# Performance work log

Hardware: AMD Instinct MI355X
Metric: run time of the kernel (lower is better)

## Reference

```python
import jax, jax.numpy as jnp
import numpy as np

N, D, S, R = 50000, 256, 6, 4
EPS = 1e-5

def group_norm1(x, w, b):
    # GroupNorm with 1 group on [N, C]: normalize each row over channels
    m = jnp.mean(x, axis=-1, keepdims=True)
    v = jnp.mean(jnp.square(x - m), axis=-1, keepdims=True)
    return (x - m) * jax.lax.rsqrt(v + EPS) * w + b

def setup_inputs() -> dict:
    key = jax.random.key(0)
    ks = jax.random.split(key, 10)
    scale = 1.0 / np.sqrt(D)
    return {
        'lane_features': jax.random.normal(ks[0], (N, D), jnp.float32),
        'W_ctr': jax.random.normal(ks[1], (R, D, D), jnp.float32) * scale,
        'norm_w': jnp.ones((R, D), jnp.float32),
        'norm_b': jnp.zeros((R, D), jnp.float32),
        'W_ctr2': jax.random.normal(ks[2], (R, D, D), jnp.float32) * scale,
        'ctr2_norm_w': jnp.ones((R, D), jnp.float32),
        'ctr2_norm_b': jnp.zeros((R, D), jnp.float32),
        'W_pre': jax.random.normal(ks[3], (R, S, D, D), jnp.float32) * scale,
        'W_suc': jax.random.normal(ks[4], (R, S, D, D), jnp.float32) * scale,
        'pre_idx': jax.random.randint(ks[5], (S, N), 0, N, jnp.int32),
        'suc_idx': jax.random.randint(ks[6], (S, N), 0, N, jnp.int32),
        'n_hop_pre': jax.random.randint(ks[7], (S, N), 0, N, jnp.int32),
        'n_hop_suc': jax.random.randint(ks[8], (S, N), 0, N, jnp.int32),
    }

def reference(lane_features, W_ctr, norm_w, norm_b, W_ctr2, ctr2_norm_w,
              ctr2_norm_b, W_pre, W_suc, pre_idx, suc_idx, n_hop_pre, n_hop_suc):
    x = lane_features
    res = x
    for i in range(R):
        # ctr linear (bias=False): x @ W.T
        temp = x @ W_ctr[i].T
        for k in range(S):
            # pre branch: gather n_hop_pre, linear, scatter-add at suc
            msg_pre = x[n_hop_pre[k]] @ W_pre[i, k].T
            temp = temp.at[suc_idx[k]].add(msg_pre)
            # suc branch: gather n_hop_suc, linear, scatter-add at pre
            msg_suc = x[n_hop_suc[k]] @ W_suc[i, k].T
            temp = temp.at[pre_idx[k]].add(msg_suc)
        x = jax.nn.relu(group_norm1(temp, norm_w[i], norm_b[i]))
        # ctr2: Linear(no bias) + GroupNorm, no activation
        x = group_norm1(x @ W_ctr2[i].T, ctr2_norm_w[i], ctr2_norm_b[i])
        x = jax.nn.relu(x + res)
        res = x
    return x
```

## Files before the change

### kernel.cpp

```cpp
#include <hip/hip_runtime.h>

#define NROWS 50000
#define DIM   256
#define SHOPS 6
#define ROUNDS 4
#define EPSV  1e-5f
#define ND ((size_t)NROWS * DIM)
#define NB  196
#define EMAXR 32768
#define EMAXND ((size_t)EMAXR * DIM)

typedef _Float16 f16x8 __attribute__((ext_vector_type(8)));
typedef _Float16 f16x4 __attribute__((ext_vector_type(4)));
typedef float    f32x4 __attribute__((ext_vector_type(4)));

#define GLDS16(GP, LP) \
    __builtin_amdgcn_global_load_lds((const __attribute__((address_space(1))) unsigned*)(GP), \
                                     (__attribute__((address_space(3))) unsigned*)(LP), 16, 0, 0)

__device__ __forceinline__ int imin(int a, int b) { return a < b ? a : b; }

__global__ __launch_bounds__(256)
void gemm_p(const _Float16* __restrict__ A, const _Float16* __restrict__ WH,
            int s0, int s1, int nz, _Float16* __restrict__ C0,
            _Float16* __restrict__ CZ, int ctr0, int nwg,
            const int* __restrict__ LIVE, const int* __restrict__ Ecnt,
            int sbase)
{
    __shared__ _Float16 lds[3][8192];
    char* ldsb = (char*)lds;

    const int bid = blockIdx.x;
    const int q   = nwg >> 3, r = nwg & 7;
    const int xcd = bid & 7,  ii = bid >> 3;
    const int g   = (xcd < r) ? xcd * (q + 1) + ii
                              : r * (q + 1) + (xcd - r) * q + ii;
    const int j   = g / (2 * nz);
    const int sub = g - j * 2 * nz;
    const int by  = sub & 1;
    const size_t z = sub >> 1;
    int xp, jj;
    if (j < 7 * 49) { xp = j / 49; jj = j % 49; }
    else            { xp = 7; jj = j - 7 * 49; }
    const int bx = jj * 8 + xp;

    const int seg = sbase + (int)z;
    const int En  = (seg >= 0) ? Ecnt[seg] : NROWS;
    const int bm0 = bx * 128;
    if (bm0 >= En) return;
    const int* lvp = (seg >= 0) ? LIVE + (size_t)seg * NROWS : nullptr;

    const int tid = threadIdx.x;
    const int l   = tid & 63;
    const int w   = tid >> 6;
    const int wm  = w & 1;
    const int wn  = w >> 1;
    const int bn0 = by * 128;
    const int lr  = l & 15;
    const int sl  = l >> 4;

    const int wslot = (z == 0) ? s0 : s1 + (int)z;
    const char* Ab = (const char*)A;
    const char* Wb = (const char*)(WH + (size_t)wslot * (DIM * DIM));

    int arow[2], slog[2], wrow[2];
    #pragma unroll
    for (int qq = 0; qq < 2; ++qq) {
        const int c   = (w * 2 + qq) * 64 + l;
        const int row = c >> 2;
        slog[qq] = (c & 3) ^ ((row >> 1) & 3);
        const int cl = imin(bm0 + row, En - 1);
        arow[qq] = lvp ? lvp[cl] : cl;
        wrow[qq] = bn0 + row;
    }

    f32x4 acc[4][4];
    #pragma unroll
    for (int mt = 0; mt < 4; ++mt)
        #pragma unroll
        for (int nt = 0; nt < 4; ++nt)
            acc[mt][nt] = (f32x4){0.f, 0.f, 0.f, 0.f};

    auto stage = [&](int step, int buf) {
        const int kt64 = step * 64;
        char* base = ldsb + buf * 16384;
        #pragma unroll
        for (int qq = 0; qq < 2; ++qq) {
            GLDS16(Ab + (size_t)arow[qq] * 512 + kt64 + slog[qq] * 16,
                   base + (w * 2 + qq) * 1024);
            GLDS16(Wb + (size_t)wrow[qq] * 512 + kt64 + slog[qq] * 16,
                   base + 8192 + (w * 2 + qq) * 1024);
        }
    };

    auto compute = [&](int buf) {
        const char* base = ldsb + buf * 16384;
        f16x8 af[4], bf[4];
        #pragma unroll
        for (int mt = 0; mt < 4; ++mt) {
            const int row = wm * 64 + mt * 16 + lr;
            af[mt] = *(const f16x8*)(base + row * 64 + ((sl ^ ((row >> 1) & 3)) << 4));
        }
        #pragma unroll
        for (int nt = 0; nt < 4; ++nt) {
            const int row = wn * 64 + nt * 16 + lr;
            bf[nt] = *(const f16x8*)(base + 8192 + row * 64 + ((sl ^ ((row >> 1) & 3)) << 4));
        }
        #pragma unroll
        for (int mt = 0; mt < 4; ++mt)
            #pragma unroll
            for (int nt = 0; nt < 4; ++nt)
                acc[mt][nt] = __builtin_amdgcn_mfma_f32_16x16x32_f16(
                    af[mt], bf[nt], acc[mt][nt], 0, 0, 0);
    };

    stage(0, 0);
    stage(1, 1);
    #pragma unroll
    for (int t = 0; t < 7; ++t) {
        asm volatile("s_waitcnt vmcnt(4)" ::: "memory");
        __builtin_amdgcn_s_barrier();
        __builtin_amdgcn_sched_barrier(0);
        if (t < 6) stage(t + 2, (t + 2) % 3);
        compute(t % 3);
    }
    asm volatile("s_waitcnt vmcnt(0)" ::: "memory");
    __builtin_amdgcn_s_barrier();
    __builtin_amdgcn_sched_barrier(0);
    compute(7 % 3);

    __syncthreads();
    _Float16* et = (_Float16*)ldsb;
    #pragma unroll
    for (int mt = 0; mt < 4; ++mt)
        #pragma unroll
        for (int nt = 0; nt < 4; ++nt)
            #pragma unroll
            for (int jv = 0; jv < 4; ++jv) {
                const int row = wm * 64 + mt * 16 + sl * 4 + jv;
                const int col = wn * 64 + nt * 16 + lr;
                et[row * 136 + col] = (_Float16)acc[mt][nt][jv];
            }
    __syncthreads();
    _Float16* Cb = (ctr0 && z == 0) ? C0 : CZ + (size_t)((int)z - ctr0) * EMAXND;
    #pragma unroll
    for (int qq = 0; qq < 8; ++qq) {
        const int c   = qq * 256 + tid;
        const int row = c >> 4;
        const int cc  = (c & 15) * 8;
        const int orow = bm0 + row;
        if (orow < En) {
            const f16x8 v = *(const f16x8*)(et + row * 136 + cc);
            *(f16x8*)(Cb + (size_t)orow * DIM + bn0 + cc) = v;
        }
    }
}

__global__ __launch_bounds__(512)
void gemm_gn(const _Float16* __restrict__ A, const _Float16* __restrict__ WH,
             int wslot, const float* __restrict__ gw, const float* __restrict__ gb,
             float* __restrict__ X, _Float16* __restrict__ Xh, int writex)
{
    __shared__ char ldsb[3 * 24576 + 4096];
    float* sArr  = (float*)(ldsb + 73728);
    float* ssArr = sArr + 512;

    const int tid = threadIdx.x;
    const int l   = tid & 63;
    const int w   = tid >> 6;
    const int wm  = w & 1;
    const int wn  = w >> 1;
    const int bm0 = blockIdx.x * 128;
    const int lr  = l & 15;
    const int sl  = l >> 4;

    const char* Ab = (const char*)A;
    const char* Wb = (const char*)(WH + (size_t)wslot * (DIM * DIM));

    int arow, aslog, wr0, ws0, wr1, ws1;
    {
        int c = tid, row = c >> 2;
        aslog = (c & 3) ^ ((row >> 1) & 3);
        arow  = imin(bm0 + row, NROWS - 1);
        ws0 = aslog; wr0 = row;
        c = tid + 512; row = c >> 2;
        ws1 = (c & 3) ^ ((row >> 1) & 3); wr1 = row;
    }

    f32x4 acc[4][4];
    #pragma unroll
    for (int mt = 0; mt < 4; ++mt)
        #pragma unroll
        for (int nt = 0; nt < 4; ++nt)
            acc[mt][nt] = (f32x4){0.f, 0.f, 0.f, 0.f};

    auto stage = [&](int step, int buf) {
        const int kt64 = step * 64;
        char* base = ldsb + buf * 24576;
        GLDS16(Ab + (size_t)arow * 512 + kt64 + aslog * 16, base + w * 1024);
        GLDS16(Wb + (size_t)wr0 * 512 + kt64 + ws0 * 16, base + 8192 + w * 1024);
        GLDS16(Wb + (size_t)wr1 * 512 + kt64 + ws1 * 16, base + 16384 + w * 1024);
    };

    auto compute = [&](int buf) {
        const char* base = ldsb + buf * 24576;
        f16x8 af[4], bf[4];
        #pragma unroll
        for (int mt = 0; mt < 4; ++mt) {
            const int row = wm * 64 + mt * 16 + lr;
            af[mt] = *(const f16x8*)(base + row * 64 + ((sl ^ ((row >> 1) & 3)) << 4));
        }
        #pragma unroll
        for (int nt = 0; nt < 4; ++nt) {
            const int row = wn * 64 + nt * 16 + lr;
            bf[nt] = *(const f16x8*)(base + 8192 + row * 64 + ((sl ^ ((row >> 1) & 3)) << 4));
        }
        #pragma unroll
        for (int mt = 0; mt < 4; ++mt)
            #pragma unroll
            for (int nt = 0; nt < 4; ++nt)
                acc[mt][nt] = __builtin_amdgcn_mfma_f32_16x16x32_f16(
                    af[mt], bf[nt], acc[mt][nt], 0, 0, 0);
    };

    stage(0, 0);
    stage(1, 1);
    #pragma unroll
    for (int t = 0; t < 7; ++t) {
        asm volatile("s_waitcnt vmcnt(3)" ::: "memory");
        __builtin_amdgcn_s_barrier();
        __builtin_amdgcn_sched_barrier(0);
        if (t < 6) stage(t + 2, (t + 2) % 3);
        compute(t % 3);
    }
    asm volatile("s_waitcnt vmcnt(0)" ::: "memory");
    __builtin_amdgcn_s_barrier();
    __builtin_amdgcn_sched_barrier(0);
    compute(7 % 3);

    float sp[4][4], ssp[4][4];
    #pragma unroll
    for (int mt = 0; mt < 4; ++mt)
        #pragma unroll
        for (int jv = 0; jv < 4; ++jv) {
            float s = 0.f, ss = 0.f;
            #pragma unroll
            for (int nt = 0; nt < 4; ++nt) {
                const float v = acc[mt][nt][jv];
                s += v; ss += v * v;
            }
            sp[mt][jv] = s; ssp[mt][jv] = ss;
        }
    #pragma unroll
    for (int off = 1; off < 16; off <<= 1)
        #pragma unroll
        for (int mt = 0; mt < 4; ++mt)
            #pragma unroll
            for (int jv = 0; jv < 4; ++jv) {
                sp[mt][jv]  += __shfl_xor(sp[mt][jv], off);
                ssp[mt][jv] += __shfl_xor(ssp[mt][jv], off);
            }
    __syncthreads();
    if (lr == 0) {
        #pragma unroll
        for (int mt = 0; mt < 4; ++mt)
            #pragma unroll
            for (int jv = 0; jv < 4; ++jv) {
                const int row = wm * 64 + mt * 16 + sl * 4 + jv;
                sArr[wn * 128 + row]  = sp[mt][jv];
                ssArr[wn * 128 + row] = ssp[mt][jv];
            }
    }
    __syncthreads();
    float mv[4][4], iv[4][4];
    #pragma unroll
    for (int mt = 0; mt < 4; ++mt)
        #pragma unroll
        for (int jv = 0; jv < 4; ++jv) {
            const int row = wm * 64 + mt * 16 + sl * 4 + jv;
            const float S  = sArr[row] + sArr[128 + row] + sArr[256 + row] + sArr[384 + row];
            const float SS = ssArr[row] + ssArr[128 + row] + ssArr[256 + row] + ssArr[384 + row];
            const float m  = S * (1.0f / DIM);
            mv[mt][jv] = m;
            iv[mt][jv] = rsqrtf(SS * (1.0f / DIM) - m * m + EPSV);
        }
    float gwv[4], gbv[4];
    #pragma unroll
    for (int nt = 0; nt < 4; ++nt) {
        const int col = wn * 64 + nt * 16 + lr;
        gwv[nt] = gw[col]; gbv[nt] = gb[col];
    }

    _Float16* et = (_Float16*)ldsb;
    #pragma unroll
    for (int half = 0; half < 2; ++half) {
        __syncthreads();
        if (wm == half) {
            #pragma unroll
            for (int mt = 0; mt < 4; ++mt)
                #pragma unroll
                for (int nt = 0; nt < 4; ++nt)
                    #pragma unroll
                    for (int jv = 0; jv < 4; ++jv) {
                        const int rl  = mt * 16 + sl * 4 + jv;
                        const int col = wn * 64 + nt * 16 + lr;
                        et[rl * 264 + col] = (_Float16)((acc[mt][nt][jv] - mv[mt][jv])
                                                        * iv[mt][jv] * gwv[nt] + gbv[nt]);
                    }
        }
        __syncthreads();
        #pragma unroll
        for (int qq = 0; qq < 4; ++qq) {
            const int c   = qq * 512 + tid;
            const int row = c >> 5;
            const int cc  = (c & 31) * 8;
            const int orow = bm0 + half * 64 + row;
            if (orow < NROWS) {
                const f16x8 y = *(const f16x8*)(et + row * 264 + cc);
                const f16x8 rr = *(const f16x8*)(Xh + (size_t)orow * DIM + cc);
                float o[8];
                #pragma unroll
                for (int e = 0; e < 8; ++e)
                    o[e] = fmaxf((float)y[e] + (float)rr[e], 0.f);
                f16x8 oh;
                #pragma unroll
                for (int e = 0; e < 8; ++e) oh[e] = (_Float16)o[e];
                *(f16x8*)(Xh + (size_t)orow * DIM + cc) = oh;
                if (writex) {
                    float* xp = X + (size_t)orow * DIM + cc;
                    *(float4*)xp       = make_float4(o[0], o[1], o[2], o[3]);
                    *(float4*)(xp + 4) = make_float4(o[4], o[5], o[6], o[7]);
                }
            }
        }
    }
}

__global__ __launch_bounds__(256)
void cvt_init(const float* __restrict__ lane, _Float16* __restrict__ Xh,
              const float* __restrict__ Wctr, const float* __restrict__ Wctr2,
              const float* __restrict__ Wpre, const float* __restrict__ Wsuc,
              _Float16* __restrict__ WH)
{
    const int bid = blockIdx.x;
    if (bid < 12500) {
        const size_t i4 = (size_t)bid * 256 + threadIdx.x;
        if (i4 >= ND / 4) return;
        const float4 v = *(const float4*)(lane + i4 * 4);
        f16x4 h;
        h[0] = (_Float16)v.x; h[1] = (_Float16)v.y;
        h[2] = (_Float16)v.z; h[3] = (_Float16)v.w;
        *(f16x4*)(Xh + i4 * 4) = h;
    } else {
        const size_t i4 = (size_t)(bid - 12500) * 256 + threadIdx.x;
        const size_t NT = (size_t)56 * DIM * DIM / 4;
        if (i4 >= NT) return;
        const size_t e = i4 * 4;
        const int slot = (int)(e >> 16);
        const int off  = (int)(e & 65535);
        const float* src;
        if (slot < 48) {
            const int r = slot / 12, s = slot % 12, k = s >> 1, dir = s & 1;
            src = (dir ? Wsuc : Wpre) + (((size_t)r * SHOPS + k) << 16) + off;
        } else if (slot < 52) {
            src = Wctr + ((size_t)(slot - 48) << 16) + off;
        } else {
            src = Wctr2 + ((size_t)(slot - 52) << 16) + off;
        }
        const float4 v = *(const float4*)src;
        f16x4 h;
        h[0] = (_Float16)v.x; h[1] = (_Float16)v.y;
        h[2] = (_Float16)v.z; h[3] = (_Float16)v.w;
        *(f16x4*)(WH + e) = h;
    }
}

__global__ __launch_bounds__(256)
void markcount(const int* __restrict__ pidx, const int* __restrict__ sidx,
               const int* __restrict__ nhp, const int* __restrict__ nhs,
               int* __restrict__ mark, int* __restrict__ counts,
               int* __restrict__ countsA)
{
    const int i = blockIdx.x * 256 + threadIdx.x;
    if (i >= NROWS) return;
    const int s = blockIdx.y;
    const int k = s >> 1, dir = s & 1;
    const int* gp  = (dir ? nhs  : nhp)  + k * NROWS;
    const int* scp = (dir ? pidx : sidx) + k * NROWS;
    mark[(size_t)s * NROWS + gp[i]] = 1;
    const int dst = scp[i];
    atomicAdd(&counts[dst], 1);
    if (s < 6) atomicAdd(&countsA[dst], 1);
}

__global__ __launch_bounds__(256)
void pscan1(const int* __restrict__ mark, const int* __restrict__ counts,
            int* __restrict__ mrank, int* __restrict__ msum,
            int* __restrict__ offs, int* __restrict__ bsum)
{
    __shared__ int wsum[4];
    const int y = blockIdx.y;
    const int tid = threadIdx.x, lane = tid & 63, wv = tid >> 6;
    const int i = blockIdx.x * 256 + tid;
    const int c = (i < NROWS) ? ((y < 12) ? mark[(size_t)y * NROWS + i] : counts[i]) : 0;
    int v = c;
    #pragma unroll
    for (int off = 1; off < 64; off <<= 1) {
        const int t = __shfl_up(v, off);
        if (lane >= off) v += t;
    }
    if (lane == 63) wsum[wv] = v;
    __syncthreads();
    int add = 0;
    for (int w = 0; w < wv; ++w) add += wsum[w];
    const int excl = add + v - c;
    if (i < NROWS) {
        if (y < 12) mrank[(size_t)y * NROWS + i] = excl;
        else        offs[i] = excl;
    }
    if (tid == 255) {
        const int tot = wsum[0] + wsum[1] + wsum[2] + wsum[3];
        if (y < 12) msum[y * 256 + blockIdx.x] = tot;
        else        bsum[blockIdx.x] = tot;
    }
}

__global__ __launch_bounds__(256)
void pscan2(const int* __restrict__ msum, const int* __restrict__ bsum,
            int* __restrict__ mbpre, int* __restrict__ bpre,
            int* __restrict__ Ecnt)
{
    __shared__ int wsum[4];
    const int y = blockIdx.x;
    const int tid = threadIdx.x, lane = tid & 63, wv = tid >> 6;
    const int c = (tid < NB) ? ((y < 12) ? msum[y * 256 + tid] : bsum[tid]) : 0;
    int v = c;
    #pragma unroll
    for (int off = 1; off < 64; off <<= 1) {
        const int t = __shfl_up(v, off);
        if (lane >= off) v += t;
    }
    if (lane == 63) wsum[wv] = v;
    __syncthreads();
    int add = 0;
    for (int w = 0; w < wv; ++w) add += wsum[w];
    if (tid < NB) {
        if (y < 12) mbpre[y * 256 + tid] = add + v - c;
        else        bpre[tid] = add + v - c;
    }
    if (tid == 0 && y < 12)
        Ecnt[y] = wsum[0] + wsum[1] + wsum[2] + wsum[3];
}

__global__ __launch_bounds__(256)
void pscan3(const int* __restrict__ mark, int* __restrict__ mrank,
            const int* __restrict__ mbpre, int* __restrict__ live,
            int* __restrict__ offs, const int* __restrict__ bpre,
            const int* __restrict__ countsA, int* __restrict__ cursorA,
            int* __restrict__ cursorB, int* __restrict__ mid)
{
    const int i = blockIdx.x * 256 + threadIdx.x;
    const int y = blockIdx.y;
    if (y < 12) {
        if (i >= NROWS) return;
        const size_t o = (size_t)y * NROWS + i;
        const int rk = mrank[o] + mbpre[y * 256 + blockIdx.x];
        mrank[o] = rk;
        if (mark[o]) live[(size_t)y * NROWS + rk] = i;
    } else {
        if (i < NROWS) {
            const int v = offs[i] + bpre[blockIdx.x];
            offs[i] = v;
            cursorA[i] = v;
            const int m = v + countsA[i];
            mid[i] = m;
            cursorB[i] = m;
        }
        if (i == 0) offs[NROWS] = 12 * NROWS;
    }
}

__global__ __launch_bounds__(256)
void fill_kernel(const int* __restrict__ pidx, const int* __restrict__ sidx,
                 const int* __restrict__ nhp, const int* __restrict__ nhs,
                 const int* __restrict__ mrank,
                 int* __restrict__ cursorA, int* __restrict__ cursorB,
                 int* __restrict__ entries)
{
    const int i = blockIdx.x * 256 + threadIdx.x;
    if (i >= NROWS) return;
    const int s = blockIdx.y;
    const int k = s >> 1, dir = s & 1;
    const int* scp = (dir ? pidx : sidx) + k * NROWS;
    const int* gp  = (dir ? nhs  : nhp)  + k * NROWS;
    const int dst = scp[i];
    const int pos = (s < 6) ? atomicAdd(&cursorA[dst], 1)
                            : atomicAdd(&cursorB[dst], 1);
    entries[pos] = (s << 16) | mrank[(size_t)s * NROWS + gp[i]];
}

#define PF 20
template<int FIRST, int LAST>
__global__ __launch_bounds__(256)
void combine_f16(const _Float16* __restrict__ YC, _Float16* __restrict__ TEMP16,
                 const _Float16* __restrict__ YB,
                 const int* __restrict__ offsets, const int* __restrict__ mid,
                 const int* __restrict__ entries,
                 int c0, int half,
                 const float* __restrict__ gw, const float* __restrict__ gb,
                 _Float16* __restrict__ Hh)
{
    const int lane = threadIdx.x & 63;
    const int wv   = threadIdx.x >> 6;
    const int r    = blockIdx.x * 4 + wv;
    if (r >= NROWS) return;
    const size_t rowoff = (size_t)r * DIM + lane * 4;

    const f16x4 ivv = FIRST ? *(const f16x4*)(YC + rowoff)
                            : *(const f16x4*)(TEMP16 + rowoff);
    float4 acc;
    acc.x = (float)ivv[0]; acc.y = (float)ivv[1];
    acc.z = (float)ivv[2]; acc.w = (float)ivv[3];

    int e0, e1;
    if (half == 0)      { e0 = offsets[r]; e1 = mid[r]; }
    else if (half == 1) { e0 = mid[r];     e1 = offsets[r + 1]; }
    else                { e0 = offsets[r]; e1 = offsets[r + 1]; }

    const int n  = e1 - e0;
    const int nf = n < PF ? n : PF;
    f16x4 buf[PF];
    #pragma unroll
    for (int t = 0; t < PF; ++t) {
        if (t < nf) {
            const int ent = entries[e0 + t];
            buf[t] = *(const f16x4*)(YB + (size_t)((ent >> 16) - c0) * EMAXND
                                     + (size_t)(ent & 0xFFFF) * DIM + lane * 4);
        }
    }
    #pragma unroll
    for (int t = 0; t < PF; ++t) {
        if (t < nf) {
            acc.x += (float)buf[t][0]; acc.y += (float)buf[t][1];
            acc.z += (float)buf[t][2]; acc.w += (float)buf[t][3];
        }
    }
    for (int e = e0 + nf; e < e1; ++e) {
        const int ent = entries[e];
        const f16x4 yv = *(const f16x4*)(YB + (size_t)((ent >> 16) - c0) * EMAXND
                                         + (size_t)(ent & 0xFFFF) * DIM + lane * 4);
        acc.x += (float)yv[0]; acc.y += (float)yv[1];
        acc.z += (float)yv[2]; acc.w += (float)yv[3];
    }

    if (LAST) {
        float s  = acc.x + acc.y + acc.z + acc.w;
        float ss = acc.x * acc.x + acc.y * acc.y + acc.z * acc.z + acc.w * acc.w;
        #pragma unroll
        for (int off = 32; off >= 1; off >>= 1) {
            s  += __shfl_xor(s, off);
            ss += __shfl_xor(ss, off);
        }
        const float m   = s * (1.0f / DIM);
        const float var = ss * (1.0f / DIM) - m * m;
        const float inv = rsqrtf(var + EPSV);
        const float4 wv4 = *(const float4*)(gw + lane * 4);
        const float4 bv4 = *(const float4*)(gb + lane * 4);
        f16x4 o;
        o[0] = (_Float16)fmaxf((acc.x - m) * inv * wv4.x + bv4.x, 0.f);
        o[1] = (_Float16)fmaxf((acc.y - m) * inv * wv4.y + bv4.y, 0.f);
        o[2] = (_Float16)fmaxf((acc.z - m) * inv * wv4.z + bv4.z, 0.f);
        o[3] = (_Float16)fmaxf((acc.w - m) * inv * wv4.w + bv4.w, 0.f);
        *(f16x4*)(Hh + rowoff) = o;
    } else {
        f16x4 o;
        o[0] = (_Float16)acc.x; o[1] = (_Float16)acc.y;
        o[2] = (_Float16)acc.z; o[3] = (_Float16)acc.w;
        *(f16x4*)(TEMP16 + rowoff) = o;
    }
}

extern "C" void kernel_launch(void* const* d_in, const int* in_sizes, int n_in,
                              void* d_out, int out_size, void* d_ws, size_t ws_size,
                              hipStream_t stream)
{
    const float* lane   = (const float*)d_in[0];
    const float* W_ctr  = (const float*)d_in[1];
    const float* norm_w = (const float*)d_in[2];
    const float* norm_b = (const float*)d_in[3];
    const float* W_ctr2 = (const float*)d_in[4];
    const float* c2w    = (const float*)d_in[5];
    const float* c2b    = (const float*)d_in[6];
    const float* W_pre  = (const float*)d_in[7];
    const float* W_suc  = (const float*)d_in[8];
    const int*   pidx   = (const int*)d_in[9];
    const int*   sidx   = (const int*)d_in[10];
    const int*   nhp    = (const int*)d_in[11];
    const int*   nhs    = (const int*)d_in[12];

    float* X = (float*)d_out;
    _Float16* YC = (_Float16*)d_out;

    char* p = (char*)d_ws;
    int* counts  = (int*)p; p += (size_t)NROWS * 4;
    int* countsA = (int*)p; p += (size_t)NROWS * 4;
    int* offsets = (int*)p; p += (size_t)(NROWS + 4) * 4;
    int* mid     = (int*)p; p += (size_t)NROWS * 4;
    int* cursorA = (int*)p; p += (size_t)NROWS * 4;
    int* cursorB = (int*)p; p += (size_t)NROWS * 4;
    int* bsum    = (int*)p; p += 256 * 4;
    int* bpre    = (int*)p; p += 256 * 4;
    int* msum    = (int*)p; p += 12 * 256 * 4;
    int* mbpre   = (int*)p; p += 12 * 256 * 4;
    int* Ecnt    = (int*)p; p += 16 * 4;
    int* entries = (int*)p; p += (size_t)12 * NROWS * 4;
    int* LIVE    = (int*)p; p += (size_t)12 * NROWS * 4;
    p = (char*)(((uintptr_t)p + 15) & ~(uintptr_t)15);
    _Float16* Xh = (_Float16*)p; p += ND * 2;
    _Float16* Hh = (_Float16*)p; p += ND * 2;
    _Float16* WH = (_Float16*)p; p += (size_t)56 * DIM * DIM * 2;
    p = (char*)(((uintptr_t)p + 255) & ~(uintptr_t)255);
    char* area = p;

    const size_t areaB = ws_size - (size_t)(area - (char*)d_ws);
    const size_t slotb = EMAXND * 2;
    int CH;
    _Float16 *T16, *YBUF;
    if (areaB >= 12 * slotb) {
        CH = 12;
        YBUF = (_Float16*)area;
        T16 = Hh;
    } else {
        CH = 6;
        T16 = (_Float16*)area;
        YBUF = T16 + ND;
    }

    int* mark  = (int*)area;
    int* mrank = mark + (size_t)12 * NROWS;

    const dim3 blk(256);
    const int  gnBlocks = (NROWS + 3) / 4;

    cvt_init<<<16084, blk, 0, stream>>>(lane, Xh, W_ctr, W_ctr2, W_pre, W_suc, WH);
    hipMemsetAsync(counts, 0, 2 * NROWS * sizeof(int), stream);
    hipMemsetAsync(mark, 0, (size_t)12 * NROWS * sizeof(int), stream);
    markcount<<<dim3(NB, 12), blk, 0, stream>>>(pidx, sidx, nhp, nhs,
                                                mark, counts, countsA);
    pscan1<<<dim3(NB, 13), blk, 0, stream>>>(mark, counts, mrank, msum, offsets, bsum);
    pscan2<<<13, blk, 0, stream>>>(msum, bsum, mbpre, bpre, Ecnt);
    pscan3<<<dim3(NB, 13), blk, 0, stream>>>(mark, mrank, mbpre, LIVE,
                                             offsets, bpre, countsA,
                                             cursorA, cursorB, mid);
    fill_kernel<<<dim3(NB, 12), blk, 0, stream>>>(pidx, sidx, nhp, nhs, mrank,
                                                  cursorA, cursorB, entries);

    for (int i = 0; i < ROUNDS; ++i) {
        if (CH == 12) {
            const int nwg = 391 * 2 * 13;
            gemm_p<<<dim3(nwg), blk, 0, stream>>>(Xh, WH, 48 + i, i * 12 - 1,
                                                  13, YC, YBUF, 1, nwg,
                                                  LIVE, Ecnt, -1);
            combine_f16<1, 1><<<gnBlocks, blk, 0, stream>>>(YC, T16, YBUF,
                offsets, mid, entries, 0, -1,
                norm_w + i * DIM, norm_b + i * DIM, Hh);
        } else {
            for (int c0 = 0; c0 < 12; c0 += 6) {
                const bool first = (c0 == 0);
                const int ctr0  = first ? 1 : 0;
                const int slots = 6 + ctr0;
                const int nwg   = 391 * 2 * slots;
                gemm_p<<<dim3(nwg), blk, 0, stream>>>(
                    Xh, WH, first ? (48 + i) : (i * 12 + c0), i * 12 + c0 - ctr0,
                    slots, YC, YBUF, ctr0, nwg, LIVE, Ecnt, c0 - ctr0);
                if (first)
                    combine_f16<1, 0><<<gnBlocks, blk, 0, stream>>>(YC, T16, YBUF,
                        offsets, mid, entries, c0, 0,
                        norm_w + i * DIM, norm_b + i * DIM, Hh);
                else
                    combine_f16<0, 1><<<gnBlocks, blk, 0, stream>>>(YC, T16, YBUF,
                        offsets, mid, entries, c0, 1,
                        norm_w + i * DIM, norm_b + i * DIM, Hh);
            }
        }
        gemm_gn<<<391, 512, 0, stream>>>(Hh, WH, 52 + i, c2w + i * DIM,
                                         c2b + i * DIM, X, Xh,
                                         (i == ROUNDS - 1) ? 1 : 0);
    }
}
```

Baseline: 950.3 us.

## Widen gemm_p tile to 128x256 with 512 threads sharing one A tile

Result: no change. 959.6 us (+1.0%).

```diff
diff --git a/kernel.cpp b/kernel.cpp
--- a/kernel.cpp
+++ b/kernel.cpp
@@ -20,25 +20,22 @@
 
 __device__ __forceinline__ int imin(int a, int b) { return a < b ? a : b; }
 
-__global__ __launch_bounds__(256)
+__global__ __launch_bounds__(512)
 void gemm_p(const _Float16* __restrict__ A, const _Float16* __restrict__ WH,
             int s0, int s1, int nz, _Float16* __restrict__ C0,
             _Float16* __restrict__ CZ, int ctr0, int nwg,
             const int* __restrict__ LIVE, const int* __restrict__ Ecnt,
             int sbase)
 {
-    __shared__ _Float16 lds[3][8192];
-    char* ldsb = (char*)lds;
+    __shared__ char ldsb[3 * 24576];
 
     const int bid = blockIdx.x;
     const int q   = nwg >> 3, r = nwg & 7;
     const int xcd = bid & 7,  ii = bid >> 3;
     const int g   = (xcd < r) ? xcd * (q + 1) + ii
                               : r * (q + 1) + (xcd - r) * q + ii;
-    const int j   = g / (2 * nz);
-    const int sub = g - j * 2 * nz;
-    const int by  = sub & 1;
-    const size_t z = sub >> 1;
+    const int j   = g / nz;
+    const size_t z = g - j * nz;
     int xp, jj;
     if (j < 7 * 49) { xp = j / 49; jj = j % 49; }
     else            { xp = 7; jj = j - 7 * 49; }
@@ -55,7 +52,6 @@
     const int w   = tid >> 6;
     const int wm  = w & 1;
     const int wn  = w >> 1;
-    const int bn0 = by * 128;
     const int lr  = l & 15;
     const int sl  = l >> 4;
 
@@ -63,15 +59,15 @@
     const char* Ab = (const char*)A;
     const char* Wb = (const char*)(WH + (size_t)wslot * (DIM * DIM));
 
-    int arow[2], slog[2], wrow[2];
-    #pragma unroll
-    for (int qq = 0; qq < 2; ++qq) {
-        const int c   = (w * 2 + qq) * 64 + l;
-        const int row = c >> 2;
-        slog[qq] = (c & 3) ^ ((row >> 1) & 3);
+    int arow, aslog, wr0, ws0, wr1, ws1;
+    {
+        int c = tid, row = c >> 2;
+        aslog = (c & 3) ^ ((row >> 1) & 3);
         const int cl = imin(bm0 + row, En - 1);
-        arow[qq] = lvp ? lvp[cl] : cl;
-        wrow[qq] = bn0 + row;
+        arow = lvp ? lvp[cl] : cl;
+        ws0 = aslog; wr0 = row;
+        c = tid + 512; row = c >> 2;
+        ws1 = (c & 3) ^ ((row >> 1) & 3); wr1 = row;
     }
 
     f32x4 acc[4][4];
@@ -83,18 +79,14 @@
 
     auto stage = [&](int step, int buf) {
         const int kt64 = step * 64;
-        char* base = ldsb + buf * 16384;
-        #pragma unroll
-        for (int qq = 0; qq < 2; ++qq) {
-            GLDS16(Ab + (size_t)arow[qq] * 512 + kt64 + slog[qq] * 16,
-                   base + (w * 2 + qq) * 1024);
-            GLDS16(Wb + (size_t)wrow[qq] * 512 + kt64 + slog[qq] * 16,
-                   base + 8192 + (w * 2 + qq) * 1024);
-        }
+        char* base = ldsb + buf * 24576;
+        GLDS16(Ab + (size_t)arow * 512 + kt64 + aslog * 16, base + w * 1024);
+        GLDS16(Wb + (size_t)wr0 * 512 + kt64 + ws0 * 16, base + 8192 + w * 1024);
+        GLDS16(Wb + (size_t)wr1 * 512 + kt64 + ws1 * 16, base + 16384 + w * 1024);
     };
 
     auto compute = [&](int buf) {
-        const char* base = ldsb + buf * 16384;
+        const char* base = ldsb + buf * 24576;
         f16x8 af[4], bf[4];
         #pragma unroll
         for (int mt = 0; mt < 4; ++mt) {
@@ -118,7 +110,7 @@
     stage(1, 1);
     #pragma unroll
     for (int t = 0; t < 7; ++t) {
-        asm volatile("s_waitcnt vmcnt(4)" ::: "memory");
+        asm volatile("s_waitcnt vmcnt(3)" ::: "memory");
         __builtin_amdgcn_s_barrier();
         __builtin_amdgcn_sched_barrier(0);
         if (t < 6) stage(t + 2, (t + 2) % 3);
@@ -129,29 +121,34 @@
     __builtin_amdgcn_sched_barrier(0);
     compute(7 % 3);
 
-    __syncthreads();
     _Float16* et = (_Float16*)ldsb;
-    #pragma unroll
-    for (int mt = 0; mt < 4; ++mt)
-        #pragma unroll
-        for (int nt = 0; nt < 4; ++nt)
+    _Float16* Cb = (ctr0 && z == 0) ? C0 : CZ + (size_t)((int)z - ctr0) * EMAXND;
+    #pragma unroll
+    for (int half = 0; half < 2; ++half) {
+        __syncthreads();
+        if (wm == half) {
             #pragma unroll
-            for (int jv = 0; jv < 4; ++jv) {
-                const int row = wm * 64 + mt * 16 + sl * 4 + jv;
-                const int col = wn * 64 + nt * 16 + lr;
-                et[row * 136 + col] = (_Float16)acc[mt][nt][jv];
+            for (int mt = 0; mt < 4; ++mt)
+                #pragma unroll
+                for (int nt = 0; nt < 4; ++nt)
+                    #pragma unroll
+                    for (int jv = 0; jv < 4; ++jv) {
+                        const int rl  = mt * 16 + sl * 4 + jv;
+                        const int col = wn * 64 + nt * 16 + lr;
+                        et[rl * 264 + col] = (_Float16)acc[mt][nt][jv];
+                    }
+        }
+        __syncthreads();
+        #pragma unroll
+        for (int qq = 0; qq < 4; ++qq) {
+            const int c   = qq * 512 + tid;
+            const int row = c >> 5;
+            const int cc  = (c & 31) * 8;
+            const int orow = bm0 + half * 64 + row;
+            if (orow < En) {
+                const f16x8 v = *(const f16x8*)(et + row * 264 + cc);
+                *(f16x8*)(Cb + (size_t)orow * DIM + cc) = v;
             }
-    __syncthreads();
-    _Float16* Cb = (ctr0 && z == 0) ? C0 : CZ + (size_t)((int)z - ctr0) * EMAXND;
-    #pragma unroll
-    for (int qq = 0; qq < 8; ++qq) {
-        const int c   = qq * 256 + tid;
-        const int row = c >> 4;
-        const int cc  = (c & 15) * 8;
-        const int orow = bm0 + row;
-        if (orow < En) {
-            const f16x8 v = *(const f16x8*)(et + row * 136 + cc);
-            *(f16x8*)(Cb + (size_t)orow * DIM + bn0 + cc) = v;
         }
     }
 }
@@ -657,8 +654,8 @@
 
     for (int i = 0; i < ROUNDS; ++i) {
         if (CH == 12) {
-            const int nwg = 391 * 2 * 13;
-            gemm_p<<<dim3(nwg), blk, 0, stream>>>(Xh, WH, 48 + i, i * 12 - 1,
+            const int nwg = 391 * 13;
+            gemm_p<<<dim3(nwg), 512, 0, stream>>>(Xh, WH, 48 + i, i * 12 - 1,
                                                   13, YC, YBUF, 1, nwg,
                                                   LIVE, Ecnt, -1);
             combine_f16<1, 1><<<gnBlocks, blk, 0, stream>>>(YC, T16, YBUF,
@@ -669,8 +666,8 @@
                 const bool first = (c0 == 0);
                 const int ctr0  = first ? 1 : 0;
                 const int slots = 6 + ctr0;
-                const int nwg   = 391 * 2 * slots;
-                gemm_p<<<dim3(nwg), blk, 0, stream>>>(
+                const int nwg   = 391 * slots;
+                gemm_p<<<dim3(nwg), 512, 0, stream>>>(
                     Xh, WH, first ? (48 + i) : (i * 12 + c0), i * 12 + c0 - ctr0,
                     slots, YC, YBUF, ctr0, nwg, LIVE, Ecnt, c0 - ctr0);
                 if (first)
```
